# Kernel tuning notes

Hardware: AMD Instinct MI355X
Metric: run time of the kernel (lower is better)

## Reference

```python
import jax, jax.numpy as jnp
import numpy as np

EMBED = 1024
HEADS = 16
HEAD_DIM = EMBED // HEADS
SEQ = 2048
BATCH = 2


def setup_inputs() -> dict:
    key = jax.random.key(0)
    ks = jax.random.split(key, 5)
    s = 1.0 / np.sqrt(EMBED)
    return {
        "x": jax.random.normal(ks[0], (BATCH, SEQ, EMBED), jnp.float32),
        "W_qkv": jax.random.uniform(ks[1], (EMBED, 3 * EMBED), jnp.float32, -s, s),
        "b_qkv": jax.random.uniform(ks[2], (3 * EMBED,), jnp.float32, -s, s),
        "W_out": jax.random.uniform(ks[3], (EMBED, EMBED), jnp.float32, -s, s),
        "b_out": jax.random.uniform(ks[4], (EMBED,), jnp.float32, -s, s),
    }


def reference(x, W_qkv, b_qkv, W_out, b_out):
    B, S, E = x.shape
    qkv = x @ W_qkv + b_qkv                      # [B,S,3E]
    q, k, v = jnp.split(qkv, 3, axis=-1)
    # [B,S,E] -> [B,H,S,D]
    def heads(t):
        return t.reshape(B, S, HEADS, HEAD_DIM).transpose(0, 2, 1, 3)
    q, k, v = heads(q), heads(k), heads(v)
    scores = jnp.einsum("bhid,bhjd->bhij", q, k) / np.sqrt(HEAD_DIM)  # [B,H,S,S]
    causal = jnp.tril(jnp.ones((S, S), bool))
    scores = jnp.where(causal[None, None], scores, -jnp.inf)
    probs = jax.nn.softmax(scores, axis=-1)
    out = jnp.einsum("bhij,bhjd->bhid", probs, v)  # [B,H,S,D]
    out = out.transpose(0, 2, 1, 3).reshape(B, S, E)
    return out @ W_out + b_out
```

## Files before the change

### kernel.cpp

```cpp
#include <hip/hip_runtime.h>
#include <hip/hip_bf16.h>
#include <cstdint>
#include <cstddef>


typedef unsigned short u16;
typedef __attribute__((ext_vector_type(8))) short short8;
typedef __attribute__((ext_vector_type(4))) short short4v;
typedef __attribute__((ext_vector_type(4))) float floatx4;

#define MFMA16(a, b, c) __builtin_amdgcn_mfma_f32_16x16x32_bf16((a), (b), (c), 0, 0, 0)

#if __has_builtin(__builtin_amdgcn_mfma_f32_16x16x16_bf16)
#define PV_MFMA(a, b, c) __builtin_amdgcn_mfma_f32_16x16x16_bf16((a), (b), (c), 0, 0, 0)
#elif __has_builtin(__builtin_amdgcn_mfma_f32_16x16x16bf16_1k)
#define PV_MFMA(a, b, c) __builtin_amdgcn_mfma_f32_16x16x16bf16_1k((a), (b), (c), 0, 0, 0)
#else
static __device__ __forceinline__ floatx4 pv_mfma_asm(short4v a, short4v b, floatx4 c) {
    asm volatile("v_mfma_f32_16x16x16_bf16 %0, %1, %2, %0" : "+v"(c) : "v"(a), "v"(b));
    return c;
}
#define PV_MFMA(a, b, c) pv_mfma_asm((a), (b), (c))
#endif

#if __has_builtin(__builtin_amdgcn_exp2f)
#define EXP2(x) __builtin_amdgcn_exp2f(x)
#else
#define EXP2(x) exp2f(x)
#endif

#define QSCALE 0.18033688011f
#define NEGINF (-__builtin_inff())

static __device__ __forceinline__ u16 f2b(float f) {
    union { float f; uint32_t u; } v; v.f = f;
    return (u16)((v.u + 0x7fffu + ((v.u >> 16) & 1u)) >> 16);
}

static __device__ __forceinline__ uint32_t pkbf(float lo, float hi) {
    union { float f; uint32_t u; } a, b; a.f = lo; b.f = hi;
    return __builtin_amdgcn_perm(b.u + 0x8000u, a.u + 0x8000u, 0x07060302u);
}

static __device__ __forceinline__ void async_cp16(const u16* g, u16* lds_wave_base) {
    __builtin_amdgcn_global_load_lds((__attribute__((address_space(1))) void*)g,
                                     (__attribute__((address_space(3))) void*)lds_wave_base,
                                     16, 0, 0);
}


__global__ __launch_bounds__(256) void k_prep(const float* __restrict__ x,
                                              const float* __restrict__ Wq,
                                              const float* __restrict__ Wo,
                                              u16* __restrict__ xb,
                                              u16* __restrict__ wqkvT,
                                              u16* __restrict__ woutT) {
    int bx = blockIdx.x, tid = threadIdx.x;
    if (bx < 2048) {
        int g = bx * 256 + tid;
        const float4* s = (const float4*)x + (size_t)g * 2;
        float4 f0 = s[0], f1 = s[1];
        uint4 r;
        r.x = pkbf(f0.x, f0.y);
        r.y = pkbf(f0.z, f0.w);
        r.z = pkbf(f1.x, f1.y);
        r.w = pkbf(f1.z, f1.w);
        *(uint4*)(xb + (size_t)g * 8) = r;
        return;
    }
    __shared__ float t[32][33];
    const float* src;
    u16* dst;
    int R, C, b;
    if (bx < 5120) { b = bx - 2048; src = Wq; dst = wqkvT; R = 1024; C = 3072; }
    else           { b = bx - 5120; src = Wo; dst = woutT; R = 1024; C = 1024; }
    int nbx = C >> 5;
    int yq = b / nbx, xq = b - yq * nbx;
    int c0 = xq * 32, r0 = yq * 32;
    int tx = tid & 31, ty = tid >> 5;
#pragma unroll
    for (int i = 0; i < 4; ++i)
        t[ty + i * 8][tx] = src[(size_t)(r0 + ty + i * 8) * C + c0 + tx];
    __syncthreads();
#pragma unroll
    for (int i = 0; i < 4; ++i)
        dst[(size_t)(c0 + ty + i * 8) * R + r0 + tx] = f2b(t[tx][ty + i * 8]);
}


__global__ __launch_bounds__(256, 3) void k_qkv_gemm(const u16* __restrict__ A,
                                                     const u16* __restrict__ Bt,
                                                     const float* __restrict__ bias,
                                                     u16* __restrict__ Qb,
                                                     u16* __restrict__ Kb,
                                                     u16* __restrict__ Vtb) {
    __shared__ __align__(16) u16 As[3][128 * 32];
    __shared__ __align__(16) u16 Bs[3][128 * 32];
    int tid = threadIdx.x;
    int w = tid >> 6, lane = tid & 63, quad = lane >> 4, l16 = lane & 15;
    int wm = w >> 1, wn = w & 1;
    int m0 = blockIdx.y * 128, n0 = blockIdx.x * 128;
    int wb = (tid & ~63) * 8;

    int ra0 = tid >> 2, ca0 = (tid & 3) * 8;
    int ra1 = (256 + tid) >> 2, ca1 = (tid & 3) * 8;
    const u16* A0 = &A[(size_t)(m0 + ra0) * 1024 + ca0];
    const u16* A1 = &A[(size_t)(m0 + ra1) * 1024 + ca1];
    const u16* B0 = &Bt[(size_t)(n0 + ra0) * 1024 + ca0];
    const u16* B1 = &Bt[(size_t)(n0 + ra1) * 1024 + ca1];

    auto stage = [&](int src_kt, int slot) {
        int ko = src_kt * 32;
        async_cp16(A0 + ko, &As[slot][wb]);
        async_cp16(A1 + ko, &As[slot][2048 + wb]);
        async_cp16(B0 + ko, &Bs[slot][wb]);
        async_cp16(B1 + ko, &Bs[slot][2048 + wb]);
    };

    floatx4 acc[4][4] = {};
    stage(0, 0);
    stage(1, 1);

    for (int kt = 0; kt < 32; ++kt) {
        asm volatile("s_waitcnt vmcnt(4)" ::: "memory");
        asm volatile("s_barrier" ::: "memory");
        int jn = kt + 2;
        stage(jn < 32 ? jn : 31, jn % 3);
        int s = kt % 3;
        short8 af[4], bf[4];
#pragma unroll
        for (int mt = 0; mt < 4; ++mt)
            af[mt] = *(const short8*)&As[s][(wm * 64 + mt * 16 + l16) * 32 + quad * 8];
#pragma unroll
        for (int nt = 0; nt < 4; ++nt)
            bf[nt] = *(const short8*)&Bs[s][(wn * 64 + nt * 16 + l16) * 32 + quad * 8];
#pragma unroll
        for (int mt = 0; mt < 4; ++mt)
#pragma unroll
            for (int nt = 0; nt < 4; ++nt)
                acc[mt][nt] = MFMA16(af[mt], bf[nt], acc[mt][nt]);
    }

    int region = n0 >> 10;
    if (region == 2) {
#pragma unroll
        for (int mt = 0; mt < 4; ++mt)
#pragma unroll
            for (int nt = 0; nt < 4; ++nt) {
                int n_abs = n0 + wn * 64 + nt * 16 + l16;
                int e = n_abs & 1023, h = e >> 6, d = e & 63;
                float vb = bias[n_abs];
                int mrow = m0 + wm * 64 + mt * 16 + quad * 4;
                int b = mrow >> 11, s0 = mrow & 2047;
                uint2 val;
                val.x = pkbf(acc[mt][nt][0] + vb, acc[mt][nt][1] + vb);
                val.y = pkbf(acc[mt][nt][2] + vb, acc[mt][nt][3] + vb);
                *(uint2*)&Vtb[((size_t)(b * 16 + h) * 64 + d) * 2048 + s0] = val;
            }
    } else {
        u16* dst = region == 0 ? Qb : Kb;
        float scl = region == 0 ? QSCALE : 1.0f;
#pragma unroll
        for (int mt = 0; mt < 4; ++mt)
#pragma unroll
            for (int nt = 0; nt < 4; ++nt)
#pragma unroll
                for (int r = 0; r < 4; ++r) {
                    int m_abs = m0 + wm * 64 + mt * 16 + quad * 4 + r;
                    int n_abs = n0 + wn * 64 + nt * 16 + l16;
                    float val = (acc[mt][nt][r] + bias[n_abs]) * scl;
                    int e = n_abs & 1023, h = e >> 6, d = e & 63;
                    int b = m_abs >> 11, s = m_abs & 2047;
                    dst[((size_t)(b * 16 + h) * 2048 + s) * 64 + d] = f2b(val);
                }
    }
}


__global__ __launch_bounds__(256, 4) void k_out_gemm(const u16* __restrict__ A,
                                                     const u16* __restrict__ Bt,
                                                     const float* __restrict__ bias,
                                                     float* __restrict__ out) {
    __shared__ __align__(16) u16 As[3][64 * 32];
    __shared__ __align__(16) u16 Bs[3][128 * 32];
    int tid = threadIdx.x;
    int w = tid >> 6, lane = tid & 63, quad = lane >> 4, l16 = lane & 15;
    int wm = w >> 1, wn = w & 1;
    int m0 = blockIdx.y * 64, n0 = blockIdx.x * 128;
    int wb = (tid & ~63) * 8;

    int ra0 = tid >> 2, ca0 = (tid & 3) * 8;
    int ra1 = (256 + tid) >> 2;
    const u16* A0 = &A[(size_t)(m0 + ra0) * 1024 + ca0];
    const u16* B0 = &Bt[(size_t)(n0 + ra0) * 1024 + ca0];
    const u16* B1 = &Bt[(size_t)(n0 + ra1) * 1024 + ca0];

    auto stage = [&](int src_kt, int slot) {
        int ko = src_kt * 32;
        async_cp16(A0 + ko, &As[slot][wb]);
        async_cp16(B0 + ko, &Bs[slot][wb]);
        async_cp16(B1 + ko, &Bs[slot][2048 + wb]);
    };

    floatx4 acc[2][4] = {};
    stage(0, 0);
    stage(1, 1);

    for (int kt = 0; kt < 32; ++kt) {
        asm volatile("s_waitcnt vmcnt(3)" ::: "memory");
        asm volatile("s_barrier" ::: "memory");
        int jn = kt + 2;
        stage(jn < 32 ? jn : 31, jn % 3);
        int s = kt % 3;
        short8 af[2], bf[4];
#pragma unroll
        for (int mt = 0; mt < 2; ++mt)
            af[mt] = *(const short8*)&As[s][(wm * 32 + mt * 16 + l16) * 32 + quad * 8];
#pragma unroll
        for (int nt = 0; nt < 4; ++nt)
            bf[nt] = *(const short8*)&Bs[s][(wn * 64 + nt * 16 + l16) * 32 + quad * 8];
#pragma unroll
        for (int mt = 0; mt < 2; ++mt)
#pragma unroll
            for (int nt = 0; nt < 4; ++nt)
                acc[mt][nt] = MFMA16(af[mt], bf[nt], acc[mt][nt]);
    }

#pragma unroll
    for (int mt = 0; mt < 2; ++mt)
#pragma unroll
        for (int nt = 0; nt < 4; ++nt)
#pragma unroll
            for (int r = 0; r < 4; ++r) {
                int m_abs = m0 + wm * 32 + mt * 16 + quad * 4 + r;
                int n_abs = n0 + wn * 64 + nt * 16 + l16;
                out[(size_t)m_abs * 1024 + n_abs] = acc[mt][nt][r] + bias[n_abs];
            }
}


__global__ __launch_bounds__(512, 4) void k_attn(const u16* __restrict__ Qb,
                                                 const u16* __restrict__ Kb,
                                                 const u16* __restrict__ Vtb,
                                                 u16* __restrict__ attnb) {
    __shared__ __align__(16) u16 KV[4][2][4096];
    int tid = threadIdx.x;
    int w = tid >> 6, lane = tid & 63, quad = lane >> 4, l16 = lane & 15;
    int L = blockIdx.x;
    int bh = ((L & 7) << 2) | ((L >> 3) & 3);
    int idx = (L >> 5) & 15;
    int tile = idx < 8 ? idx : 23 - idx;
    const u16* Qp = Qb + (size_t)bh * 131072;
    const u16* Kp = Kb + (size_t)bh * 131072;
    const u16* Vp = Vtb + (size_t)bh * 131072;
    int b = bh >> 4, h = bh & 15;

    int r0 = tid >> 3, c0 = ((tid & 7) ^ (r0 & 7)) * 8;
    int kOff = r0 * 64 + c0;
    int vOff = r0 * 2048 + c0;
    int wb = (tid & ~63) * 8;

    int g  = w >> 2;
    int wq = w & 3;
    int q_a = tile * 128 + wq * 32 + l16;
    int q_b = q_a + 16;
    short8 qa0 = *(const short8*)&Qp[(size_t)q_a * 64 + quad * 8];
    short8 qa1 = *(const short8*)&Qp[(size_t)q_a * 64 + 32 + quad * 8];
    short8 qb0 = *(const short8*)&Qp[(size_t)q_b * 64 + quad * 8];
    short8 qb1 = *(const short8*)&Qp[(size_t)q_b * 64 + 32 + quad * 8];

    int n = 2 * tile + 2;
    int lastk = 2 * tile + (wq >> 1);

    auto stage = [&](int j) {
        u16* Ks = (u16*)KV[j & 3][0];
        u16* Vs = (u16*)KV[j & 3][1];
        async_cp16(Kp + (size_t)j * 4096 + kOff, Ks + wb);
        async_cp16(Vp + (size_t)j * 64 + vOff, Vs + wb);
    };

    floatx4 acc[2][4] = {};
    float lp[2] = {0.f, 0.f};
    int sw = l16 & 7;

    stage(0); stage(1); stage(2);

    for (int kt = 0; kt < n; ++kt) {
        asm volatile("s_waitcnt vmcnt(4)" ::: "memory");
        asm volatile("s_barrier" ::: "memory");
        {
            int jn = kt + 3;
            stage(jn < n ? jn : n - 1);
        }
        if (kt <= lastk) {
            const u16* Ks = (const u16*)KV[kt & 3][0];
            const u16* Vs = (const u16*)KV[kt & 3][1];

            short8 kfa[2], kfb[2];
#pragma unroll
            for (int nt = 0; nt < 2; ++nt) {
                int rb = (g * 32 + nt * 16 + l16) * 8;
                kfa[nt] = *(const short8*)&Ks[(rb + (quad ^ sw)) * 8];
                kfb[nt] = *(const short8*)&Ks[(rb + ((4 + quad) ^ sw)) * 8];
            }
            short4v vf[2][4];
#pragma unroll
            for (int dt = 0; dt < 4; ++dt) {
                const char* rowb = (const char*)Vs + (dt * 16 + l16) * 128 + (quad & 1) * 8;
#pragma unroll
                for (int nt = 0; nt < 2; ++nt) {
                    int chunk = g * 4 + nt * 2 + (quad >> 1);
                    vf[nt][dt] = *(const short4v*)(rowb + ((chunk ^ sw) * 16));
                }
            }

            floatx4 sa[2][2] = {};
            __builtin_amdgcn_s_setprio(1);
#pragma unroll
            for (int nt = 0; nt < 2; ++nt) {
                sa[0][nt] = MFMA16(kfa[nt], qa0, sa[0][nt]);
                sa[0][nt] = MFMA16(kfb[nt], qa1, sa[0][nt]);
                sa[1][nt] = MFMA16(kfa[nt], qb0, sa[1][nt]);
                sa[1][nt] = MFMA16(kfb[nt], qb1, sa[1][nt]);
            }
            __builtin_amdgcn_s_setprio(0);
            if (kt == lastk) {
#pragma unroll
                for (int nt = 0; nt < 2; ++nt)
#pragma unroll
                    for (int r = 0; r < 4; ++r) {
                        int key = kt * 64 + g * 32 + nt * 16 + quad * 4 + r;
                        if (key > q_a) sa[0][nt][r] = NEGINF;
                        if (key > q_b) sa[1][nt][r] = NEGINF;
                    }
            }
            float p[2][2][4];
#pragma unroll
            for (int rb = 0; rb < 2; ++rb)
#pragma unroll
                for (int nt = 0; nt < 2; ++nt)
#pragma unroll
                    for (int r = 0; r < 4; ++r)
                        p[rb][nt][r] = EXP2(sa[rb][nt][r]);
#pragma unroll
            for (int rb = 0; rb < 2; ++rb) {
                float s0 = (p[rb][0][0] + p[rb][0][1]) + (p[rb][0][2] + p[rb][0][3]);
                float s1 = (p[rb][1][0] + p[rb][1][1]) + (p[rb][1][2] + p[rb][1][3]);
                lp[rb] += s0 + s1;
            }
            union { uint2 u; short4v s; } pf[2][2];
#pragma unroll
            for (int rb = 0; rb < 2; ++rb)
#pragma unroll
                for (int nt = 0; nt < 2; ++nt) {
                    pf[rb][nt].u.x = pkbf(p[rb][nt][0], p[rb][nt][1]);
                    pf[rb][nt].u.y = pkbf(p[rb][nt][2], p[rb][nt][3]);
                }
            __builtin_amdgcn_s_setprio(1);
#pragma unroll
            for (int rb = 0; rb < 2; ++rb)
#pragma unroll
                for (int nt = 0; nt < 2; ++nt)
#pragma unroll
                    for (int dt = 0; dt < 4; ++dt)
                        acc[rb][dt] = PV_MFMA(vf[nt][dt], pf[rb][nt].s, acc[rb][dt]);
            __builtin_amdgcn_s_setprio(0);
        }
    }

    asm volatile("s_waitcnt vmcnt(0)" ::: "memory");
    __syncthreads();
    float* scr  = (float*)KV;
    float* lscr = scr + 128 * 64;
    if (g == 1) {
#pragma unroll
        for (int rb = 0; rb < 2; ++rb) {
            int ql = wq * 32 + rb * 16 + l16;
#pragma unroll
            for (int dt = 0; dt < 4; ++dt)
                *(floatx4*)&scr[ql * 64 + dt * 16 + quad * 4] = acc[rb][dt];
            float lr1 = lp[rb];
            lr1 += __shfl_xor(lr1, 16);
            lr1 += __shfl_xor(lr1, 32);
            lscr[ql] = lr1;
        }
    }
    __syncthreads();
    if (g == 0) {
#pragma unroll
        for (int rb = 0; rb < 2; ++rb) {
            int ql = wq * 32 + rb * 16 + l16;
            float lr = lp[rb];
            lr += __shfl_xor(lr, 16);
            lr += __shfl_xor(lr, 32);
            lr += lscr[ql];
            float inv = 1.f / lr;
            size_t base = ((size_t)(b * 2048 + tile * 128 + ql)) * 1024 + h * 64;
#pragma unroll
            for (int dt = 0; dt < 4; ++dt) {
                floatx4 o = acc[rb][dt] + *(const floatx4*)&scr[ql * 64 + dt * 16 + quad * 4];
                uint2 val;
                val.x = pkbf(o[0] * inv, o[1] * inv);
                val.y = pkbf(o[2] * inv, o[3] * inv);
                *(uint2*)&attnb[base + dt * 16 + quad * 4] = val;
            }
        }
    }
}


extern "C" void kernel_launch(void* const* d_in, const int* in_sizes, int n_in,
                              void* d_out, int out_size, void* d_ws, size_t ws_size,
                              hipStream_t stream) {
    const float* x     = (const float*)d_in[0];
    const float* W_qkv = (const float*)d_in[1];
    const float* b_qkv = (const float*)d_in[2];
    const float* W_out = (const float*)d_in[3];
    const float* b_out = (const float*)d_in[4];
    float* out = (float*)d_out;

    char* p = (char*)d_ws;
    u16* xb    = (u16*)p; p += (size_t)4096 * 1024 * 2;
    u16* wqkvT = (u16*)p; p += (size_t)3072 * 1024 * 2;
    u16* woutT = (u16*)p; p += (size_t)1024 * 1024 * 2;
    u16* Qb    = (u16*)p; p += (size_t)32 * 2048 * 64 * 2;
    u16* Kb    = (u16*)p; p += (size_t)32 * 2048 * 64 * 2;
    u16* Vtb   = (u16*)p; p += (size_t)32 * 64 * 2048 * 2;
    u16* attnb = xb;

    k_prep<<<6144, 256, 0, stream>>>(x, W_qkv, W_out, xb, wqkvT, woutT);
    k_qkv_gemm<<<dim3(24, 32), 256, 0, stream>>>(xb, wqkvT, b_qkv, Qb, Kb, Vtb);
    k_attn<<<512, 512, 0, stream>>>(Qb, Kb, Vtb, attnb);
    k_out_gemm<<<dim3(8, 64), 256, 0, stream>>>(attnb, woutT, b_out, out);
}
```

Before: 173.9 us.

## Load K/V fragments directly from global memory instead of LDS pipeline

Removes the four-stage async-copy shared-memory pipeline for K and V tiles in the attention kernel; each wave now reads its MFMA fragments directly from global memory and loops only up to its own last causal tile. This eliminates per-tile barriers and most LDS usage, possibly raising occupancy. In exchange, K/V data is re-read by every wave from cache, V reads are strided and poorly coalesced, and load latency is no longer overlapped with compute.

Result: slower. 232.3 us (+33.6%).

```diff
diff --git a/kernel.cpp b/kernel.cpp
--- a/kernel.cpp
+++ b/kernel.cpp
@@ -243,7 +243,7 @@
                                                  const u16* __restrict__ Kb,
                                                  const u16* __restrict__ Vtb,
                                                  u16* __restrict__ attnb) {
-    __shared__ __align__(16) u16 KV[4][2][4096];
+    __shared__ float scr[128 * 64 + 128];
     int tid = threadIdx.x;
     int w = tid >> 6, lane = tid & 63, quad = lane >> 4, l16 = lane & 15;
     int L = blockIdx.x;
@@ -255,11 +255,6 @@
     const u16* Vp = Vtb + (size_t)bh * 131072;
     int b = bh >> 4, h = bh & 15;
 
-    int r0 = tid >> 3, c0 = ((tid & 7) ^ (r0 & 7)) * 8;
-    int kOff = r0 * 64 + c0;
-    int vOff = r0 * 2048 + c0;
-    int wb = (tid & ~63) * 8;
-
     int g  = w >> 2;
     int wq = w & 3;
     int q_a = tile * 128 + wq * 32 + l16;
@@ -269,108 +264,84 @@
     short8 qb0 = *(const short8*)&Qp[(size_t)q_b * 64 + quad * 8];
     short8 qb1 = *(const short8*)&Qp[(size_t)q_b * 64 + 32 + quad * 8];
 
-    int n = 2 * tile + 2;
     int lastk = 2 * tile + (wq >> 1);
-
-    auto stage = [&](int j) {
-        u16* Ks = (u16*)KV[j & 3][0];
-        u16* Vs = (u16*)KV[j & 3][1];
-        async_cp16(Kp + (size_t)j * 4096 + kOff, Ks + wb);
-        async_cp16(Vp + (size_t)j * 64 + vOff, Vs + wb);
-    };
 
     floatx4 acc[2][4] = {};
     float lp[2] = {0.f, 0.f};
-    int sw = l16 & 7;
-
-    stage(0); stage(1); stage(2);
-
-    for (int kt = 0; kt < n; ++kt) {
-        asm volatile("s_waitcnt vmcnt(4)" ::: "memory");
-        asm volatile("s_barrier" ::: "memory");
-        {
-            int jn = kt + 3;
-            stage(jn < n ? jn : n - 1);
-        }
-        if (kt <= lastk) {
-            const u16* Ks = (const u16*)KV[kt & 3][0];
-            const u16* Vs = (const u16*)KV[kt & 3][1];
-
-            short8 kfa[2], kfb[2];
+
+    for (int kt = 0; kt <= lastk; ++kt) {
+        const u16* kbase = Kp + (size_t)(kt * 64 + g * 32) * 64;
+        short8 kfa[2], kfb[2];
+#pragma unroll
+        for (int nt = 0; nt < 2; ++nt) {
+            const u16* krow = kbase + (nt * 16 + l16) * 64;
+            kfa[nt] = *(const short8*)&krow[quad * 8];
+            kfb[nt] = *(const short8*)&krow[32 + quad * 8];
+        }
+        const u16* vbase = Vp + (size_t)kt * 64 + g * 32;
+        short4v vf[2][4];
+#pragma unroll
+        for (int dt = 0; dt < 4; ++dt) {
+            const u16* vrow = vbase + (size_t)(dt * 16 + l16) * 2048;
+#pragma unroll
+            for (int nt = 0; nt < 2; ++nt)
+                vf[nt][dt] = *(const short4v*)&vrow[nt * 16 + quad * 4];
+        }
+
+        floatx4 sa[2][2] = {};
+        __builtin_amdgcn_s_setprio(1);
+#pragma unroll
+        for (int nt = 0; nt < 2; ++nt) {
+            sa[0][nt] = MFMA16(kfa[nt], qa0, sa[0][nt]);
+            sa[0][nt] = MFMA16(kfb[nt], qa1, sa[0][nt]);
+            sa[1][nt] = MFMA16(kfa[nt], qb0, sa[1][nt]);
+            sa[1][nt] = MFMA16(kfb[nt], qb1, sa[1][nt]);
+        }
+        __builtin_amdgcn_s_setprio(0);
+        if (kt == lastk) {
+#pragma unroll
+            for (int nt = 0; nt < 2; ++nt)
+#pragma unroll
+                for (int r = 0; r < 4; ++r) {
+                    int key = kt * 64 + g * 32 + nt * 16 + quad * 4 + r;
+                    if (key > q_a) sa[0][nt][r] = NEGINF;
+                    if (key > q_b) sa[1][nt][r] = NEGINF;
+                }
+        }
+        float p[2][2][4];
+#pragma unroll
+        for (int rb = 0; rb < 2; ++rb)
+#pragma unroll
+            for (int nt = 0; nt < 2; ++nt)
+#pragma unroll
+                for (int r = 0; r < 4; ++r)
+                    p[rb][nt][r] = EXP2(sa[rb][nt][r]);
+#pragma unroll
+        for (int rb = 0; rb < 2; ++rb) {
+            float s0 = (p[rb][0][0] + p[rb][0][1]) + (p[rb][0][2] + p[rb][0][3]);
+            float s1 = (p[rb][1][0] + p[rb][1][1]) + (p[rb][1][2] + p[rb][1][3]);
+            lp[rb] += s0 + s1;
+        }
+        union { uint2 u; short4v s; } pf[2][2];
+#pragma unroll
+        for (int rb = 0; rb < 2; ++rb)
 #pragma unroll
             for (int nt = 0; nt < 2; ++nt) {
-                int rb = (g * 32 + nt * 16 + l16) * 8;
-                kfa[nt] = *(const short8*)&Ks[(rb + (quad ^ sw)) * 8];
-                kfb[nt] = *(const short8*)&Ks[(rb + ((4 + quad) ^ sw)) * 8];
+                pf[rb][nt].u.x = pkbf(p[rb][nt][0], p[rb][nt][1]);
+                pf[rb][nt].u.y = pkbf(p[rb][nt][2], p[rb][nt][3]);
             }
-            short4v vf[2][4];
-#pragma unroll
-            for (int dt = 0; dt < 4; ++dt) {
-                const char* rowb = (const char*)Vs + (dt * 16 + l16) * 128 + (quad & 1) * 8;
-#pragma unroll
-                for (int nt = 0; nt < 2; ++nt) {
-                    int chunk = g * 4 + nt * 2 + (quad >> 1);
-                    vf[nt][dt] = *(const short4v*)(rowb + ((chunk ^ sw) * 16));
-                }
-            }
-
-            floatx4 sa[2][2] = {};
-            __builtin_amdgcn_s_setprio(1);
-#pragma unroll
-            for (int nt = 0; nt < 2; ++nt) {
-                sa[0][nt] = MFMA16(kfa[nt], qa0, sa[0][nt]);
-                sa[0][nt] = MFMA16(kfb[nt], qa1, sa[0][nt]);
-                sa[1][nt] = MFMA16(kfa[nt], qb0, sa[1][nt]);
-                sa[1][nt] = MFMA16(kfb[nt], qb1, sa[1][nt]);
-            }
-            __builtin_amdgcn_s_setprio(0);
-            if (kt == lastk) {
-#pragma unroll
-                for (int nt = 0; nt < 2; ++nt)
-#pragma unroll
-                    for (int r = 0; r < 4; ++r) {
-                        int key = kt * 64 + g * 32 + nt * 16 + quad * 4 + r;
-                        if (key > q_a) sa[0][nt][r] = NEGINF;
-                        if (key > q_b) sa[1][nt][r] = NEGINF;
-                    }
-            }
-            float p[2][2][4];
-#pragma unroll
-            for (int rb = 0; rb < 2; ++rb)
-#pragma unroll
-                for (int nt = 0; nt < 2; ++nt)
-#pragma unroll
-                    for (int r = 0; r < 4; ++r)
-                        p[rb][nt][r] = EXP2(sa[rb][nt][r]);
-#pragma unroll
-            for (int rb = 0; rb < 2; ++rb) {
-                float s0 = (p[rb][0][0] + p[rb][0][1]) + (p[rb][0][2] + p[rb][0][3]);
-                float s1 = (p[rb][1][0] + p[rb][1][1]) + (p[rb][1][2] + p[rb][1][3]);
-                lp[rb] += s0 + s1;
-            }
-            union { uint2 u; short4v s; } pf[2][2];
-#pragma unroll
-            for (int rb = 0; rb < 2; ++rb)
-#pragma unroll
-                for (int nt = 0; nt < 2; ++nt) {
-                    pf[rb][nt].u.x = pkbf(p[rb][nt][0], p[rb][nt][1]);
-                    pf[rb][nt].u.y = pkbf(p[rb][nt][2], p[rb][nt][3]);
-                }
-            __builtin_amdgcn_s_setprio(1);
-#pragma unroll
-            for (int rb = 0; rb < 2; ++rb)
-#pragma unroll
-                for (int nt = 0; nt < 2; ++nt)
-#pragma unroll
-                    for (int dt = 0; dt < 4; ++dt)
-                        acc[rb][dt] = PV_MFMA(vf[nt][dt], pf[rb][nt].s, acc[rb][dt]);
-            __builtin_amdgcn_s_setprio(0);
-        }
-    }
-
-    asm volatile("s_waitcnt vmcnt(0)" ::: "memory");
-    __syncthreads();
-    float* scr  = (float*)KV;
+        __builtin_amdgcn_s_setprio(1);
+#pragma unroll
+        for (int rb = 0; rb < 2; ++rb)
+#pragma unroll
+            for (int nt = 0; nt < 2; ++nt)
+#pragma unroll
+                for (int dt = 0; dt < 4; ++dt)
+                    acc[rb][dt] = PV_MFMA(vf[nt][dt], pf[rb][nt].s, acc[rb][dt]);
+        __builtin_amdgcn_s_setprio(0);
+    }
+
+    float* oscr = scr;
     float* lscr = scr + 128 * 64;
     if (g == 1) {
 #pragma unroll
@@ -378,7 +349,7 @@
             int ql = wq * 32 + rb * 16 + l16;
 #pragma unroll
             for (int dt = 0; dt < 4; ++dt)
-                *(floatx4*)&scr[ql * 64 + dt * 16 + quad * 4] = acc[rb][dt];
+                *(floatx4*)&oscr[ql * 64 + dt * 16 + quad * 4] = acc[rb][dt];
             float lr1 = lp[rb];
             lr1 += __shfl_xor(lr1, 16);
             lr1 += __shfl_xor(lr1, 32);
@@ -398,7 +369,7 @@
             size_t base = ((size_t)(b * 2048 + tile * 128 + ql)) * 1024 + h * 64;
 #pragma unroll
             for (int dt = 0; dt < 4; ++dt) {
-                floatx4 o = acc[rb][dt] + *(const floatx4*)&scr[ql * 64 + dt * 16 + quad * 4];
+                floatx4 o = acc[rb][dt] + *(const floatx4*)&oscr[ql * 64 + dt * 16 + quad * 4];
                 uint2 val;
                 val.x = pkbf(o[0] * inv, o[1] * inv);
                 val.y = pkbf(o[2] * inv, o[3] * inv);
```
